# Performance work log

Hardware: AMD Instinct MI355X
Metric: run time of the kernel (lower is better)

The kernel has to match this reference:

```python
import math
import jax, jax.numpy as jnp
import numpy as np

B, S, D, H, M, R = 4, 2048, 512, 8, 4, 32
HD = D // H
EPS = 1e-8


def setup_inputs() -> dict:
    key = jax.random.key(0)
    ks = jax.random.split(key, 12)
    sc = 1.0 / math.sqrt(D)
    return {
        "x": jax.random.normal(ks[0], (B, S, D), jnp.float32),
        "Wq": jax.random.normal(ks[1], (D, D), jnp.float32) * sc,
        "bq": jnp.zeros((D,), jnp.float32),
        "Wk": jax.random.normal(ks[2], (D, D), jnp.float32) * sc,
        "bk": jnp.zeros((D,), jnp.float32),
        "Wv": jax.random.normal(ks[3], (D, D), jnp.float32) * sc,
        "bv": jnp.zeros((D,), jnp.float32),
        "mask1": jax.random.normal(ks[4], (M, R, S), jnp.float32) * (1.0 / math.sqrt(R)),
        "mask2": jax.random.normal(ks[5], (M, R, S), jnp.float32) * (1.0 / math.sqrt(R)),
        "Wo": jax.random.normal(ks[6], (D, D), jnp.float32) * sc,
        "bo": jnp.zeros((D,), jnp.float32),
        "roll_back": jax.random.randint(ks[7], (1, S, S), 0, S, jnp.int32),
    }


def reference(x, Wq, bq, Wk, bk, Wv, bv, mask1, mask2, Wo, bo, roll_back):
    # q, k, v: [B, H, S, HD]  (torch Linear: x @ W.T + b)
    def proj(W, b):
        return (x @ W.T + b).reshape(B, S, H, HD).transpose(0, 2, 1, 3)
    q, k, v = proj(Wq, bq), proj(Wk, bk), proj(Wv, bv)

    # learnable_mask[m,s,t] = sum_r mask1[m,r,s] * mask2[m,r,t]  -> [M, S, S]
    lm = jnp.einsum("mrs,mrt->mst", mask1, mask2)
    # gather along last dim with roll indices expanded to [M, S, S]
    idx = jnp.broadcast_to(roll_back, lm.shape)
    lm_rolled = jnp.take_along_axis(lm, idx, axis=-1)  # [M, S, S]

    # att: [B, H, S, S]
    att = jnp.einsum("bhsd,bhtd->bhst", q, k) / math.sqrt(HD)
    # group heads: [B, H/M, M, S, S] * [1, 1, M, S, S]
    att = att.reshape(B, H // M, M, S, S) * lm_rolled[None, None]
    att = att.reshape(B, H, S, S)

    # Frobenius norm over last two dims, per (batch, head)
    fro = jnp.sqrt(jnp.sum(att * att, axis=(-2, -1), keepdims=True))
    att = att / (fro + EPS)

    out = jnp.einsum("bhst,bhtd->bshd", att, v).reshape(B, S, D)
    return out @ Wo.T + bo
```

## Files before the change

### kernel.cpp

```cpp
#include <hip/hip_runtime.h>
#include <hip/hip_bf16.h>

#define NB 4
#define NS 2048
#define ND 512
#define NH 8
#define NM 4
#define NR 32
#define NHD 64

typedef short frag_ab __attribute__((ext_vector_type(8)));
typedef float frag_cd __attribute__((ext_vector_type(4)));

__device__ __forceinline__ float bf2f(short s) {
    union { unsigned u; float f; } c;
    c.u = ((unsigned)(unsigned short)s) << 16;
    return c.f;
}
__device__ __forceinline__ short f2bf(float f) {
    __hip_bfloat16 h = __float2bfloat16(f);
    union { __hip_bfloat16 h; short s; } c;
    c.h = h;
    return c.s;
}

__device__ __forceinline__ void gload16(const void* g, void* l) {
    __builtin_amdgcn_global_load_lds((const __attribute__((address_space(1))) unsigned int*)g,
                                     (__attribute__((address_space(3))) unsigned int*)l,
                                     16, 0, 0);
}

__device__ __forceinline__ void stage_tile(const short* src, size_t srcStride,
                                           char* lbase, int slot) {
    int o = slot * 16;
    int row = o >> 7;
    int cc = ((o >> 4) & 7) ^ (row & 7);
    gload16(src + (size_t)row * srcStride + cc * 8, lbase + o);
}

__device__ __forceinline__ frag_ab lds_frag(const char* lbase, int row, int cc_un) {
    int cc = cc_un ^ (row & 7);
    return *(const frag_ab*)(lbase + row * 128 + cc * 16);
}

__global__ void __launch_bounds__(256) k_cast(const float* __restrict__ in,
                                              short* __restrict__ out, int n8) {
    int i = blockIdx.x * 256 + threadIdx.x;
    if (i >= n8) return;
    const float4* p = (const float4*)in + (size_t)i * 2;
    float4 a = p[0], b = p[1];
    frag_ab o;
    o[0] = f2bf(a.x); o[1] = f2bf(a.y); o[2] = f2bf(a.z); o[3] = f2bf(a.w);
    o[4] = f2bf(b.x); o[5] = f2bf(b.y); o[6] = f2bf(b.z); o[7] = f2bf(b.w);
    ((frag_ab*)out)[i] = o;
}

__global__ void __launch_bounds__(256) k_castw(const float* __restrict__ Wq,
                                               const float* __restrict__ Wk,
                                               const float* __restrict__ Wv,
                                               const float* __restrict__ Wo,
                                               short* __restrict__ out) {
    int i = blockIdx.x * 256 + threadIdx.x;
    int which = i >> 15;
    int j = i & 32767;
    const float* src = which == 0 ? Wq : which == 1 ? Wk : which == 2 ? Wv : Wo;
    const float4* p = (const float4*)src + (size_t)j * 2;
    float4 a = p[0], b = p[1];
    frag_ab o;
    o[0] = f2bf(a.x); o[1] = f2bf(a.y); o[2] = f2bf(a.z); o[3] = f2bf(a.w);
    o[4] = f2bf(b.x); o[5] = f2bf(b.y); o[6] = f2bf(b.z); o[7] = f2bf(b.w);
    ((frag_ab*)out)[i] = o;
}

__global__ void __launch_bounds__(256) k_tcast_mask(const float* __restrict__ mask1,
                                                    const float* __restrict__ mask2,
                                                    short* __restrict__ m1t,
                                                    short* __restrict__ m2t) {
    int my = blockIdx.y;
    const float* in = my < 4 ? mask1 : mask2;
    short* out = my < 4 ? m1t : m2t;
    int m = my & 3;
    int s0 = blockIdx.x * 64, tid = threadIdx.x;
    __shared__ float tile[32][65];
    int c = tid & 63, r4 = tid >> 6;
#pragma unroll
    for (int p = 0; p < 8; ++p) {
        int r = p * 4 + r4;
        tile[r][c] = in[(m * 32 + r) * NS + s0 + c];
    }
    __syncthreads();
    int r = tid & 31, s4 = tid >> 5;
#pragma unroll
    for (int p = 0; p < 8; ++p) {
        int s = p * 8 + s4;
        out[(m * NS + s0 + s) * NR + r] = f2bf(tile[r][s]);
    }
}

__global__ void __launch_bounds__(64) k_lm(const short* __restrict__ m1t,
                                           const short* __restrict__ m2t,
                                           short* __restrict__ lm) {
    int tb = blockIdx.x * 64, sb = blockIdx.y * 64, m = blockIdx.z;
    int lane = threadIdx.x;
    int lo = lane & 15, g = lane >> 4;
    frag_ab a[4], b[4];
#pragma unroll
    for (int i = 0; i < 4; ++i) {
        a[i] = *(const frag_ab*)(m1t + (m * NS + sb + i * 16 + lo) * NR + g * 8);
        b[i] = *(const frag_ab*)(m2t + (m * NS + tb + i * 16 + lo) * NR + g * 8);
    }
#pragma unroll
    for (int mi = 0; mi < 4; ++mi)
#pragma unroll
        for (int ni = 0; ni < 4; ++ni) {
            frag_cd z = {0.f, 0.f, 0.f, 0.f};
            frag_cd d = __builtin_amdgcn_mfma_f32_16x16x32_bf16(a[mi], b[ni], z, 0, 0, 0);
#pragma unroll
            for (int r = 0; r < 4; ++r) {
                int srow = sb + mi * 16 + g * 4 + r;
                int tcol = tb + ni * 16 + lo;
                lm[(size_t)(m * NS + srow) * NS + tcol] = f2bf(d[r]);
            }
        }
}

__global__ void __launch_bounds__(256) k_roll(const short* __restrict__ lm,
                                              const int* __restrict__ roll,
                                              short* __restrict__ lmr) {
    int bid = blockIdx.x;
    int m = bid & 3, s = bid >> 2;
    __shared__ __align__(16) short row[NS];
    int tid = threadIdx.x;
    size_t base = (size_t)(m * NS + s) * NS;
    *(frag_ab*)(row + tid * 8) = *(const frag_ab*)(lm + base + tid * 8);
    __syncthreads();
    const int* rrow = roll + (size_t)s * NS;
    int t0 = tid * 8;
    int4 r0 = *(const int4*)(rrow + t0);
    int4 r1 = *(const int4*)(rrow + t0 + 4);
    frag_ab o;
    o[0] = row[r0.x]; o[1] = row[r0.y]; o[2] = row[r0.z]; o[3] = row[r0.w];
    o[4] = row[r1.x]; o[5] = row[r1.y]; o[6] = row[r1.z]; o[7] = row[r1.w];
    *(frag_ab*)(lmr + base + t0) = o;
}

__global__ void __launch_bounds__(256) k_gemm_qkv(const short* __restrict__ A,
                                                  const short* __restrict__ Wqb,
                                                  const short* __restrict__ Wkb,
                                                  const short* __restrict__ Wvb,
                                                  const float* __restrict__ bq,
                                                  const float* __restrict__ bk,
                                                  const float* __restrict__ bv,
                                                  short* __restrict__ Qb,
                                                  short* __restrict__ Kb,
                                                  short* __restrict__ Vtb) {
    int n = blockIdx.x;
    int rr = n >> 3;
    int Mb = (n & 7) * 8 + (rr & 7);
    int Nb = rr >> 3;
    int which = Nb >> 3;
    int bn0 = (Nb & 7) * 64;
    const short* W = which == 0 ? Wqb : which == 1 ? Wkb : Wvb;
    const float* bias = which == 0 ? bq : which == 1 ? bk : bv;
    short* out = which == 0 ? Qb : which == 1 ? Kb : Vtb;
    int bm0 = Mb * 128;
    int tid = threadIdx.x;
    int wid = tid >> 6, lane = tid & 63;
    int lo = lane & 15, g = lane >> 4;
    int wr = (wid >> 1) * 64, wc = (wid & 1) * 32;

    __shared__ __align__(16) char sm[2][24576];

    frag_cd acc[4][2];
#pragma unroll
    for (int mi = 0; mi < 4; ++mi)
#pragma unroll
        for (int ni = 0; ni < 2; ++ni) acc[mi][ni] = (frag_cd){0.f, 0.f, 0.f, 0.f};

    const short* Abase = A + (size_t)bm0 * ND;
    const short* Wbase = W + (size_t)bn0 * ND;

#pragma unroll
    for (int j = 0; j < 4; ++j) stage_tile(Abase, ND, sm[0], tid + j * 256);
#pragma unroll
    for (int j = 0; j < 2; ++j) stage_tile(Wbase, ND, sm[0] + 16384, tid + j * 256);
    __syncthreads();

    char* cb = sm[0];
    char* nb = sm[1];
    for (int kt = 0; kt < 8; ++kt) {
        if (kt < 7) {
            int k0 = (kt + 1) * 64;
#pragma unroll
            for (int j = 0; j < 4; ++j) stage_tile(Abase + k0, ND, nb, tid + j * 256);
#pragma unroll
            for (int j = 0; j < 2; ++j) stage_tile(Wbase + k0, ND, nb + 16384, tid + j * 256);
        }
#pragma unroll
        for (int kk = 0; kk < 2; ++kk) {
            frag_ab af[4], bf[2];
#pragma unroll
            for (int mi = 0; mi < 4; ++mi) af[mi] = lds_frag(cb, wr + mi * 16 + lo, kk * 4 + g);
#pragma unroll
            for (int ni = 0; ni < 2; ++ni) bf[ni] = lds_frag(cb + 16384, wc + ni * 16 + lo, kk * 4 + g);
#pragma unroll
            for (int mi = 0; mi < 4; ++mi)
#pragma unroll
                for (int ni = 0; ni < 2; ++ni)
                    acc[mi][ni] = __builtin_amdgcn_mfma_f32_16x16x32_bf16(af[mi], bf[ni], acc[mi][ni], 0, 0, 0);
        }
        __syncthreads();
        char* t = cb; cb = nb; nb = t;
    }

#pragma unroll
    for (int mi = 0; mi < 4; ++mi)
#pragma unroll
        for (int ni = 0; ni < 2; ++ni)
#pragma unroll
            for (int ri = 0; ri < 4; ++ri) {
                int row = bm0 + wr + mi * 16 + g * 4 + ri;
                int col = bn0 + wc + ni * 16 + lo;
                float v = acc[mi][ni][ri] + bias[col];
                int b = row >> 11, s = row & 2047, h = col >> 6, d = col & 63;
                if (which < 2) {
                    out[(((size_t)(b * NH + h) * NS + s) << 6) + d] = f2bf(v);
                } else {
                    out[((size_t)(b * NH + h) * NHD + d) * NS + s] = f2bf(v);
                }
            }
}

__global__ void __launch_bounds__(256) k_gemm_out(const short* __restrict__ A,
                                                  const short* __restrict__ W,
                                                  const float* __restrict__ bias,
                                                  float* __restrict__ out) {
    int n = blockIdx.x;
    int rr = n >> 3;
    int Mb = (n & 7) * 8 + (rr & 7);
    int Nb = rr >> 3;
    int bn0 = Nb * 64;
    int bm0 = Mb * 128;
    int tid = threadIdx.x;
    int wid = tid >> 6, lane = tid & 63;
    int lo = lane & 15, g = lane >> 4;
    int wr = (wid >> 1) * 64, wc = (wid & 1) * 32;

    __shared__ __align__(16) char sm[2][24576];

    frag_cd acc[4][2];
#pragma unroll
    for (int mi = 0; mi < 4; ++mi)
#pragma unroll
        for (int ni = 0; ni < 2; ++ni) acc[mi][ni] = (frag_cd){0.f, 0.f, 0.f, 0.f};

    const short* Abase = A + (size_t)bm0 * ND;
    const short* Wbase = W + (size_t)bn0 * ND;

#pragma unroll
    for (int j = 0; j < 4; ++j) stage_tile(Abase, ND, sm[0], tid + j * 256);
#pragma unroll
    for (int j = 0; j < 2; ++j) stage_tile(Wbase, ND, sm[0] + 16384, tid + j * 256);
    __syncthreads();

    char* cb = sm[0];
    char* nb = sm[1];
    for (int kt = 0; kt < 8; ++kt) {
        if (kt < 7) {
            int k0 = (kt + 1) * 64;
#pragma unroll
            for (int j = 0; j < 4; ++j) stage_tile(Abase + k0, ND, nb, tid + j * 256);
#pragma unroll
            for (int j = 0; j < 2; ++j) stage_tile(Wbase + k0, ND, nb + 16384, tid + j * 256);
        }
#pragma unroll
        for (int kk = 0; kk < 2; ++kk) {
            frag_ab af[4], bf[2];
#pragma unroll
            for (int mi = 0; mi < 4; ++mi) af[mi] = lds_frag(cb, wr + mi * 16 + lo, kk * 4 + g);
#pragma unroll
            for (int ni = 0; ni < 2; ++ni) bf[ni] = lds_frag(cb + 16384, wc + ni * 16 + lo, kk * 4 + g);
#pragma unroll
            for (int mi = 0; mi < 4; ++mi)
#pragma unroll
                for (int ni = 0; ni < 2; ++ni)
                    acc[mi][ni] = __builtin_amdgcn_mfma_f32_16x16x32_bf16(af[mi], bf[ni], acc[mi][ni], 0, 0, 0);
        }
        __syncthreads();
        char* t = cb; cb = nb; nb = t;
    }

#pragma unroll
    for (int mi = 0; mi < 4; ++mi)
#pragma unroll
        for (int ni = 0; ni < 2; ++ni)
#pragma unroll
            for (int ri = 0; ri < 4; ++ri) {
                int row = bm0 + wr + mi * 16 + g * 4 + ri;
                int col = bn0 + wc + ni * 16 + lo;
                out[(size_t)row * ND + col] = acc[mi][ni][ri] + bias[col];
            }
}

__global__ void __launch_bounds__(512) k_attn(const short* __restrict__ Qb,
                                              const short* __restrict__ Kb,
                                              const short* __restrict__ Vt,
                                              const short* __restrict__ lmr,
                                              short* __restrict__ O,
                                              float* __restrict__ fro) {
    int n = blockIdx.x;
    int xcd = n & 7;
    int idx = n >> 3;
    int b = idx & 3;
    int hh = (idx >> 2) & 1;
    int sbl = idx >> 3;
    int m = xcd >> 1;
    int sb = (xcd & 1) * 8 + sbl;
    int h = hh * 4 + m;
    int bh = b * NH + h;
    int tid = threadIdx.x;
    int w = tid >> 6, lane = tid & 63;
    int lo = lane & 15, g = lane >> 4;
    int srow = sb * 128 + w * 16;

    __shared__ __align__(16) char kv[2][16384];
    __shared__ __align__(16) short plds[8][1024];
    char* pbase = (char*)&plds[w][0];

    const short* kbase = Kb + (size_t)bh * NS * NHD;
    const short* vbase = Vt + (size_t)bh * NHD * NS;
    const short* lmbase = lmr + ((size_t)m * NS + srow + lo) * NS;

    const short* qptr = Qb + ((size_t)bh * NS + srow + lo) * NHD + g * 8;
    frag_ab qf[2];
    qf[0] = *(const frag_ab*)(qptr);
    qf[1] = *(const frag_ab*)(qptr + 32);

    frag_cd acco[4];
#pragma unroll
    for (int ni = 0; ni < 4; ++ni) acco[ni] = (frag_cd){0.f, 0.f, 0.f, 0.f};
    float sumsq = 0.f;

    stage_tile(kbase, NHD, kv[0], tid);
    stage_tile(vbase, NS, kv[0] + 8192, tid);
    frag_ab lc0 = *(const frag_ab*)(lmbase + g * 8);
    frag_ab lc1 = *(const frag_ab*)(lmbase + 32 + g * 8);
    __syncthreads();

    char* cb = kv[0];
    char* nb = kv[1];
    for (int tb = 0; tb < 32; ++tb) {
        int t0 = tb * 64;
        frag_ab ln0 = lc0, ln1 = lc1;
        if (tb < 31) {
            stage_tile(kbase + (size_t)(t0 + 64) * NHD, NHD, nb, tid);
            stage_tile(vbase + (t0 + 64), NS, nb + 8192, tid);
            ln0 = *(const frag_ab*)(lmbase + t0 + 64 + g * 8);
            ln1 = *(const frag_ab*)(lmbase + t0 + 96 + g * 8);
        }
        frag_cd sacc[4];
#pragma unroll
        for (int ni = 0; ni < 4; ++ni) sacc[ni] = (frag_cd){0.f, 0.f, 0.f, 0.f};
#pragma unroll
        for (int kk = 0; kk < 2; ++kk)
#pragma unroll
            for (int ni = 0; ni < 4; ++ni)
                sacc[ni] = __builtin_amdgcn_mfma_f32_16x16x32_bf16(
                    qf[kk], lds_frag(cb, ni * 16 + lo, kk * 4 + g), sacc[ni], 0, 0, 0);
#pragma unroll
        for (int ni = 0; ni < 4; ++ni)
#pragma unroll
            for (int r = 0; r < 4; ++r) {
                int rs = g * 4 + r;
                int ct = ni * 16 + lo;
                int byte = (rs * 128 + ct * 2) ^ ((rs & 7) << 4);
                *(short*)(pbase + byte) = f2bf(sacc[ni][r]);
            }
        frag_ab pf[2];
#pragma unroll
        for (int kk = 0; kk < 2; ++kk) {
            int rbyte = (lo * 128 + kk * 64 + g * 16) ^ ((lo & 7) << 4);
            frag_ab sf = *(const frag_ab*)(pbase + rbyte);
            frag_ab lf = kk ? lc1 : lc0;
            frag_ab pp;
#pragma unroll
            for (int j = 0; j < 8; ++j) {
                float p = bf2f(sf[j]) * bf2f(lf[j]) * 0.125f;
                sumsq += p * p;
                pp[j] = f2bf(p);
            }
            pf[kk] = pp;
        }
#pragma unroll
        for (int ni = 0; ni < 4; ++ni)
#pragma unroll
            for (int kk = 0; kk < 2; ++kk)
                acco[ni] = __builtin_amdgcn_mfma_f32_16x16x32_bf16(
                    pf[kk], lds_frag(cb + 8192, ni * 16 + lo, kk * 4 + g), acco[ni], 0, 0, 0);
        lc0 = ln0;
        lc1 = ln1;
        __syncthreads();
        char* t = cb; cb = nb; nb = t;
    }
#pragma unroll
    for (int off = 32; off; off >>= 1) sumsq += __shfl_xor(sumsq, off, 64);
    if (lane == 0) atomicAdd(&fro[bh], sumsq);
#pragma unroll
    for (int ni = 0; ni < 4; ++ni)
#pragma unroll
        for (int r = 0; r < 4; ++r) {
            int s = srow + g * 4 + r;
            int d = ni * 16 + lo;
            O[((size_t)(b * NS + s)) * ND + h * NHD + d] = f2bf(acco[ni][r]);
        }
}

__global__ void __launch_bounds__(256) k_scale(short* __restrict__ O,
                                               const float* __restrict__ fro) {
    int i = blockIdx.x * 256 + threadIdx.x;
    int i8 = i * 8;
    int col = i8 & 511;
    int row = i8 >> 9;
    float f = fro[(row >> 11) * NH + (col >> 6)];
    float sc = 1.f / (sqrtf(f) + 1e-8f);
    frag_ab v = ((frag_ab*)O)[i];
    frag_ab o;
#pragma unroll
    for (int j = 0; j < 8; ++j) o[j] = f2bf(bf2f(v[j]) * sc);
    ((frag_ab*)O)[i] = o;
}

extern "C" void kernel_launch(void* const* d_in, const int* in_sizes, int n_in,
                              void* d_out, int out_size, void* d_ws, size_t ws_size,
                              hipStream_t stream) {
    const float* x     = (const float*)d_in[0];
    const float* Wq    = (const float*)d_in[1];
    const float* bq    = (const float*)d_in[2];
    const float* Wk    = (const float*)d_in[3];
    const float* bk    = (const float*)d_in[4];
    const float* Wv    = (const float*)d_in[5];
    const float* bv    = (const float*)d_in[6];
    const float* mask1 = (const float*)d_in[7];
    const float* mask2 = (const float*)d_in[8];
    const float* Wo    = (const float*)d_in[9];
    const float* bo    = (const float*)d_in[10];
    const int*   roll  = (const int*)d_in[11];
    float* out = (float*)d_out;

    char* ws = (char*)d_ws;
    short* xb  = (short*)(ws + 0);
    short* Wqb = (short*)(ws + 8388608);
    short* Wkb = (short*)(ws + 8912896);
    short* Wvb = (short*)(ws + 9437184);
    short* Wob = (short*)(ws + 9961472);
    short* Qb  = (short*)(ws + 10485760);
    short* Kb  = (short*)(ws + 18874368);
    short* Vtb = (short*)(ws + 27262976);
    short* m1t = (short*)(ws + 35651584);
    short* m2t = (short*)(ws + 36175872);
    short* lm  = (short*)(ws + 36700160);
    short* lmr = (short*)(ws + 70254592);
    short* Ob  = (short*)(ws + 103809024);
    float* fro = (float*)(ws + 112197632);

    k_cast<<<2048, 256, 0, stream>>>(x, xb, (NB * NS * ND) / 8);
    k_castw<<<512, 256, 0, stream>>>(Wq, Wk, Wv, Wo, Wqb);
    k_tcast_mask<<<dim3(32, 8), 256, 0, stream>>>(mask1, mask2, m1t, m2t);

    k_lm<<<dim3(32, 32, 4), 64, 0, stream>>>(m1t, m2t, lm);
    k_roll<<<8192, 256, 0, stream>>>(lm, roll, lmr);

    k_gemm_qkv<<<1536, 256, 0, stream>>>(xb, Wqb, Wkb, Wvb, bq, bk, bv, Qb, Kb, Vtb);

    hipMemsetAsync(fro, 0, 128, stream);
    k_attn<<<512, 512, 0, stream>>>(Qb, Kb, Vtb, lmr, Ob, fro);

    k_scale<<<2048, 256, 0, stream>>>(Ob, fro);
    k_gemm_out<<<512, 256, 0, stream>>>(Ob, Wob, bo, out);
}
```

Before: 252.9 us.

## Fuse low-rank mask build with roll gather and keep scores fp32 in LDS

```diff
diff --git a/kernel.cpp b/kernel.cpp
--- a/kernel.cpp
+++ b/kernel.cpp
@@ -97,51 +97,55 @@
     }
 }
 
-__global__ void __launch_bounds__(64) k_lm(const short* __restrict__ m1t,
-                                           const short* __restrict__ m2t,
-                                           short* __restrict__ lm) {
-    int tb = blockIdx.x * 64, sb = blockIdx.y * 64, m = blockIdx.z;
-    int lane = threadIdx.x;
+__global__ void __launch_bounds__(256) k_lmroll(const short* __restrict__ m1t,
+                                                const short* __restrict__ m2t,
+                                                const int* __restrict__ roll,
+                                                short* __restrict__ lmr) {
+    int n = blockIdx.x;
+    int xcd = n & 7, j = n >> 3;
+    int m = xcd >> 1;
+    int st = (j << 1) | (xcd & 1);
+    int s0 = st * 16;
+    int tid = threadIdx.x, w = tid >> 6, lane = tid & 63;
     int lo = lane & 15, g = lane >> 4;
-    frag_ab a[4], b[4];
-#pragma unroll
-    for (int i = 0; i < 4; ++i) {
-        a[i] = *(const frag_ab*)(m1t + (m * NS + sb + i * 16 + lo) * NR + g * 8);
-        b[i] = *(const frag_ab*)(m2t + (m * NS + tb + i * 16 + lo) * NR + g * 8);
-    }
-#pragma unroll
-    for (int mi = 0; mi < 4; ++mi)
+
+    __shared__ __align__(16) char rowbuf_[16 * 4160];
+
+    frag_ab af = *(const frag_ab*)(m1t + (size_t)(m * NS + s0 + lo) * NR + g * 8);
+    const short* m2b = m2t + (size_t)m * NS * NR;
+
+    for (int tt = 0; tt < 8; ++tt) {
+        int T0 = (w * 8 + tt) * 64;
+        frag_cd sacc[4];
 #pragma unroll
         for (int ni = 0; ni < 4; ++ni) {
+            frag_ab bf = *(const frag_ab*)(m2b + (size_t)(T0 + ni * 16 + lo) * NR + g * 8);
             frag_cd z = {0.f, 0.f, 0.f, 0.f};
-            frag_cd d = __builtin_amdgcn_mfma_f32_16x16x32_bf16(a[mi], b[ni], z, 0, 0, 0);
-#pragma unroll
-            for (int r = 0; r < 4; ++r) {
-                int srow = sb + mi * 16 + g * 4 + r;
-                int tcol = tb + ni * 16 + lo;
-                lm[(size_t)(m * NS + srow) * NS + tcol] = f2bf(d[r]);
-            }
-        }
-}
-
-__global__ void __launch_bounds__(256) k_roll(const short* __restrict__ lm,
-                                              const int* __restrict__ roll,
-                                              short* __restrict__ lmr) {
-    int bid = blockIdx.x;
-    int m = bid & 3, s = bid >> 2;
-    __shared__ __align__(16) short row[NS];
-    int tid = threadIdx.x;
-    size_t base = (size_t)(m * NS + s) * NS;
-    *(frag_ab*)(row + tid * 8) = *(const frag_ab*)(lm + base + tid * 8);
+            sacc[ni] = __builtin_amdgcn_mfma_f32_16x16x32_bf16(af, bf, z, 0, 0, 0);
+        }
+        char* pw = rowbuf_ + g * (4 * 4160) + (size_t)(T0 + lo) * 2;
+#pragma unroll
+        for (int ni = 0; ni < 4; ++ni)
+#pragma unroll
+            for (int r = 0; r < 4; ++r)
+                *(short*)(pw + r * 4160 + ni * 32) = f2bf(sacc[ni][r]);
+    }
     __syncthreads();
-    const int* rrow = roll + (size_t)s * NS;
-    int t0 = tid * 8;
-    int4 r0 = *(const int4*)(rrow + t0);
-    int4 r1 = *(const int4*)(rrow + t0 + 4);
-    frag_ab o;
-    o[0] = row[r0.x]; o[1] = row[r0.y]; o[2] = row[r0.z]; o[3] = row[r0.w];
-    o[4] = row[r1.x]; o[5] = row[r1.y]; o[6] = row[r1.z]; o[7] = row[r1.w];
-    *(frag_ab*)(lmr + base + t0) = o;
+    int row = w * 4 + (lane >> 4);
+    int tbase = (lane & 15) * 8;
+    const short* rb = (const short*)(rowbuf_ + row * 4160);
+    const int* rrow = roll + (size_t)(s0 + row) * NS;
+    short* orow = lmr + ((size_t)(m * NS) + s0 + row) * NS;
+#pragma unroll
+    for (int c = 0; c < 16; ++c) {
+        int t = c * 128 + tbase;
+        int4 i0 = *(const int4*)(rrow + t);
+        int4 i1 = *(const int4*)(rrow + t + 4);
+        frag_ab o;
+        o[0] = rb[i0.x]; o[1] = rb[i0.y]; o[2] = rb[i0.z]; o[3] = rb[i0.w];
+        o[4] = rb[i1.x]; o[5] = rb[i1.y]; o[6] = rb[i1.z]; o[7] = rb[i1.w];
+        *(frag_ab*)(orow + t) = o;
+    }
 }
 
 __global__ void __launch_bounds__(256) k_gemm_qkv(const short* __restrict__ A,
@@ -222,6 +226,7 @@
                 int row = bm0 + wr + mi * 16 + g * 4 + ri;
                 int col = bn0 + wc + ni * 16 + lo;
                 float v = acc[mi][ni][ri] + bias[col];
+                if (which == 0) v *= 0.125f;
                 int b = row >> 11, s = row & 2047, h = col >> 6, d = col & 63;
                 if (which < 2) {
                     out[(((size_t)(b * NH + h) * NS + s) << 6) + d] = f2bf(v);
@@ -302,12 +307,12 @@
             }
 }
 
-__global__ void __launch_bounds__(512) k_attn(const short* __restrict__ Qb,
-                                              const short* __restrict__ Kb,
-                                              const short* __restrict__ Vt,
-                                              const short* __restrict__ lmr,
-                                              short* __restrict__ O,
-                                              float* __restrict__ fro) {
+__global__ void __launch_bounds__(512, 4) k_attn(const short* __restrict__ Qb,
+                                                 const short* __restrict__ Kb,
+                                                 const short* __restrict__ Vt,
+                                                 const short* __restrict__ lmr,
+                                                 short* __restrict__ O,
+                                                 float* __restrict__ fro) {
     int n = blockIdx.x;
     int xcd = n & 7;
     int idx = n >> 3;
@@ -324,8 +329,8 @@
     int srow = sb * 128 + w * 16;
 
     __shared__ __align__(16) char kv[2][16384];
-    __shared__ __align__(16) short plds[8][1024];
-    char* pbase = (char*)&plds[w][0];
+    __shared__ __align__(16) char plds[8][4352];
+    char* pbase = plds[w];
 
     const short* kbase = Kb + (size_t)bh * NS * NHD;
     const short* vbase = Vt + (size_t)bh * NHD * NS;
@@ -346,6 +351,9 @@
     frag_ab lc0 = *(const frag_ab*)(lmbase + g * 8);
     frag_ab lc1 = *(const frag_ab*)(lmbase + 32 + g * 8);
     __syncthreads();
+
+    float* pw = (float*)(pbase + g * 1088 + lo * 4);
+    const char* prb = pbase + lo * 272 + g * 32;
 
     char* cb = kv[0];
     char* nb = kv[1];
@@ -370,24 +378,21 @@
 #pragma unroll
         for (int ni = 0; ni < 4; ++ni)
 #pragma unroll
-            for (int r = 0; r < 4; ++r) {
-                int rs = g * 4 + r;
-                int ct = ni * 16 + lo;
-                int byte = (rs * 128 + ct * 2) ^ ((rs & 7) << 4);
-                *(short*)(pbase + byte) = f2bf(sacc[ni][r]);
-            }
+            for (int r = 0; r < 4; ++r)
+                pw[r * 68 + ni * 16] = sacc[ni][r];
         frag_ab pf[2];
 #pragma unroll
         for (int kk = 0; kk < 2; ++kk) {
-            int rbyte = (lo * 128 + kk * 64 + g * 16) ^ ((lo & 7) << 4);
-            frag_ab sf = *(const frag_ab*)(pbase + rbyte);
+            float4 s0 = *(const float4*)(prb + kk * 128);
+            float4 s1 = *(const float4*)(prb + kk * 128 + 16);
             frag_ab lf = kk ? lc1 : lc0;
+            float pv[8] = {s0.x, s0.y, s0.z, s0.w, s1.x, s1.y, s1.z, s1.w};
             frag_ab pp;
 #pragma unroll
-            for (int j = 0; j < 8; ++j) {
-                float p = bf2f(sf[j]) * bf2f(lf[j]) * 0.125f;
-                sumsq += p * p;
-                pp[j] = f2bf(p);
+            for (int jj = 0; jj < 8; ++jj) {
+                float p = pv[jj] * bf2f(lf[jj]);
+                sumsq = fmaf(p, p, sumsq);
+                pp[jj] = f2bf(p);
             }
             pf[kk] = pp;
         }
@@ -458,7 +463,6 @@
     short* Vtb = (short*)(ws + 27262976);
     short* m1t = (short*)(ws + 35651584);
     short* m2t = (short*)(ws + 36175872);
-    short* lm  = (short*)(ws + 36700160);
     short* lmr = (short*)(ws + 70254592);
     short* Ob  = (short*)(ws + 103809024);
     float* fro = (float*)(ws + 112197632);
@@ -467,8 +471,7 @@
     k_castw<<<512, 256, 0, stream>>>(Wq, Wk, Wv, Wo, Wqb);
     k_tcast_mask<<<dim3(32, 8), 256, 0, stream>>>(mask1, mask2, m1t, m2t);
 
-    k_lm<<<dim3(32, 32, 4), 64, 0, stream>>>(m1t, m2t, lm);
-    k_roll<<<8192, 256, 0, stream>>>(lm, roll, lmr);
+    k_lmroll<<<512, 256, 0, stream>>>(m1t, m2t, roll, lmr);
 
     k_gemm_qkv<<<1536, 256, 0, stream>>>(xb, Wqb, Wkb, Wvb, bq, bk, bv, Qb, Kb, Vtb);
 
```

After: 232.3 us. 8.1% less time.
